# Performance work log

Measured on AMD Instinct MI355X. Metric: run time of the kernel, lower is better.

The kernel has to match this reference:

```python
import jax, jax.numpy as jnp
import numpy as np

B, P, D = 16, 512, 1024   # batch, num wordpieces, bert_dim (roberta-large)
W, T, E = 400, 32, 64     # num words, num triggers (spans), num entities (spans)
H = 600                   # hidden_num of role_idn_ffn


def _make_idxs(rng, b, m, n, max_len):
    # [start, end) intervals with 0 <= start < end <= n, sorted starts per row
    starts = np.sort(rng.integers(0, n - 1, size=(b, m)), axis=1)
    ends = np.minimum(starts + rng.integers(1, max_len + 1, size=(b, m)), n)
    ends = np.maximum(ends, starts + 1)
    return np.stack([starts, ends], axis=-1).astype(np.int32)


def setup_inputs() -> dict:
    key = jax.random.key(0)
    k1, k2, k3 = jax.random.split(key, 3)
    rng = np.random.default_rng(0)
    return {
        "piece_reprs": jax.random.normal(k1, (B, P, D), dtype=jnp.float32),
        "word_idxs": jnp.asarray(_make_idxs(rng, B, W, P, 4)),
        "trigger_idxs": jnp.asarray(_make_idxs(rng, B, T, W, 8)),
        "entity_idxs": jnp.asarray(_make_idxs(rng, B, E, W, 12)),
        "W0": jax.random.normal(k2, (4 * D, H), dtype=jnp.float32) * 0.02,
        "b0": jnp.zeros((H,), dtype=jnp.float32),
        "W1": jax.random.normal(k3, (H, 2), dtype=jnp.float32) * 0.02,
        "b1": jnp.zeros((2,), dtype=jnp.float32),
    }


def _segment_mean(x, idxs):
    """Mean of x[b, start:end] per interval. x: [B,N,Dm], idxs: [B,M,2] -> [B,M,Dm].
    Vectorized replacement of the nested-loop slice+mean via inclusive prefix sums."""
    cs = jnp.concatenate([jnp.zeros_like(x[:, :1]), jnp.cumsum(x, axis=1)], axis=1)  # [B,N+1,Dm]
    s = jnp.take_along_axis(cs, idxs[:, :, 0:1], axis=1)  # [B,M,Dm]
    e = jnp.take_along_axis(cs, idxs[:, :, 1:2], axis=1)  # [B,M,Dm]
    lens = (idxs[:, :, 1] - idxs[:, :, 0]).astype(x.dtype)[:, :, None]
    return (e - s) / lens


def reference(piece_reprs, word_idxs, trigger_idxs, entity_idxs, W0, b0, W1, b1):
    # encode(): wordpiece -> word averaging (compute_word_reps_avg)
    word_reprs = _segment_mean(piece_reprs, word_idxs)          # [B, W, D]
    # scores(): span mean pooling (compute_span_reprs)
    trig = _segment_mean(word_reprs, trigger_idxs)              # [B, T, D]
    ent = _segment_mean(word_reprs, entity_idxs)                # [B, E, D]
    b, t, d = trig.shape
    e = ent.shape[1]
    # compute_binary_reprs: all (trigger, entity) pairs, trigger index varies slowly
    t_rep = jnp.broadcast_to(trig[:, :, None, :], (b, t, e, d)).reshape(b, t * e, d)
    e_rep = jnp.broadcast_to(ent[:, None, :, :], (b, t, e, d)).reshape(b, t * e, d)
    role = jnp.concatenate([t_rep, e_rep, t_rep * e_rep, jnp.abs(t_rep - e_rep)], axis=-1)  # [B,T*E,4D]
    # role_idn_ffn: Linears([4D, H, 2]) with relu between layers (dropout=0 at eval)
    h = jax.nn.relu(role @ W0 + b0)
    return h @ W1 + b1                                          # [B, T*E, 2]
```

## Files before the change

kernel.cpp:

```cpp
#include <hip/hip_runtime.h>
#include <cstddef>
#include <cstdint>

typedef float f32x4 __attribute__((ext_vector_type(4)));
typedef __bf16 bf16x8 __attribute__((ext_vector_type(8)));

constexpr int NB = 16;
constexpr int NP = 512;
constexpr int ND = 1024;
constexpr int NW = 400;
constexpr int NT = 32;
constexpr int NE = 64;
constexpr int NH = 600;
constexpr int IMGP = 128 * 64;
constexpr int IMGQ = 320 * 32;
constexpr int PREZ_N = NB * NT * NH + NB * NE * NH;

__device__ inline bf16x8 pack8(float a0, float a1, float a2, float a3,
                               float a4, float a5, float a6, float a7) {
    bf16x8 v;
    v[0] = (__bf16)a0; v[1] = (__bf16)a1; v[2] = (__bf16)a2; v[3] = (__bf16)a3;
    v[4] = (__bf16)a4; v[5] = (__bf16)a5; v[6] = (__bf16)a6; v[7] = (__bf16)a7;
    return v;
}

__device__ inline void dma16(const void* g, void* l) {
    __builtin_amdgcn_global_load_lds(
        (const __attribute__((address_space(1))) uint32_t*)g,
        (__attribute__((address_space(3))) uint32_t*)l, 16, 0, 0);
}

#define LGKM_BARRIER() \
    asm volatile("s_waitcnt lgkmcnt(0)\n\ts_barrier" ::: "memory")

template <int MAXW>
__device__ inline float4 span_mean_cols(const float* __restrict__ pbase,
                                        const int* __restrict__ wrow,
                                        int s, int e) {
    int nw = e - s;
    int ps[MAXW], pe[MAXW];
#pragma unroll
    for (int w = 0; w < MAXW; ++w) {
        bool act = w < nw;
        int ww = s + w;
        ps[w] = act ? wrow[2 * ww] : 0;
        pe[w] = act ? wrow[2 * ww + 1] : 0;
    }
    float4 acc = make_float4(0.f, 0.f, 0.f, 0.f);
#pragma unroll
    for (int cb = 0; cb < MAXW; cb += 4) {
#pragma unroll
        for (int w = cb; w < cb + 4; ++w) {
            float4 wa = make_float4(0.f, 0.f, 0.f, 0.f);
#pragma unroll
            for (int p = 0; p < 4; ++p) {
                if (ps[w] + p < pe[w]) {
                    float4 v =
                        *(const float4*)(pbase + (size_t)(ps[w] + p) * ND);
                    wa.x += v.x; wa.y += v.y; wa.z += v.z; wa.w += v.w;
                }
            }
            if (pe[w] > ps[w]) {
                float wi = 1.0f / (float)(pe[w] - ps[w]);
                acc.x += wa.x * wi; acc.y += wa.y * wi;
                acc.z += wa.z * wi; acc.w += wa.w * wi;
            }
        }
    }
    return acc;
}

__global__ __launch_bounds__(256) void prep_kernel(
    const float* __restrict__ piece, const int* __restrict__ widx,
    const int* __restrict__ tidx, const int* __restrict__ eidx,
    const float* __restrict__ W0, __bf16* __restrict__ W0pre,
    __bf16* __restrict__ W0pair, float* __restrict__ trig,
    float* __restrict__ ent, float* __restrict__ prez,
    float* __restrict__ out, int out_size) {
    __shared__ float T[32][132];
    int id = blockIdx.x;
    int t = threadIdx.x;
    if (id < NB * (NT + NE)) {
        const int* idx;
        float* outp;
        int b;
        bool is_trig = id < NB * NT;
        if (is_trig) {
            b = id / NT; idx = tidx + id * 2; outp = trig + (size_t)id * ND;
        } else {
            int id2 = id - NB * NT;
            b = id2 / NE; idx = eidx + id2 * 2; outp = ent + (size_t)id2 * ND;
        }
        int s = idx[0], e = idx[1];
        int col = t * 4;
        const int* wrow = widx + b * NW * 2;
        const float* pbase = piece + (size_t)b * NP * ND + col;
        float4 acc = is_trig ? span_mean_cols<8>(pbase, wrow, s, e)
                             : span_mean_cols<12>(pbase, wrow, s, e);
        float inv = 1.0f / (float)(e - s);
        acc.x *= inv; acc.y *= inv; acc.z *= inv; acc.w *= inv;
        *(float4*)(outp + col) = acc;
    } else if (id < NB * (NT + NE) + 704) {
        int bid = id - NB * (NT + NE);
        if (bid < 160) {
            int kb = bid & 31, nc = bid >> 5;
            __bf16* img = W0pre + ((size_t)nc * 32 + kb) * IMGP;
#pragma unroll
            for (int h = 0; h < 2; ++h) {
                {
                    int kl = t >> 3;
                    int n0 = (t & 7) * 16;
                    int kg = kb * 64 + h * 32 + kl;
                    const float* src = W0 + (size_t)kg * NH + nc * 128 + n0;
#pragma unroll
                    for (int g = 0; g < 4; ++g) {
                        int n = nc * 128 + n0 + g * 4;
                        float4 v = (n < NH) ? *(const float4*)(src + g * 4)
                                            : make_float4(0.f, 0.f, 0.f, 0.f);
                        *(float4*)&T[kl][n0 + g * 4] = v;
                    }
                }
                __syncthreads();
#pragma unroll
                for (int s = 0; s < 2; ++s) {
                    int idx = s * 256 + t;
                    int row = idx >> 2, cl = idx & 3, c = h * 4 + cl;
                    bf16x8 v = pack8(T[cl * 8 + 0][row], T[cl * 8 + 1][row],
                                     T[cl * 8 + 2][row], T[cl * 8 + 3][row],
                                     T[cl * 8 + 4][row], T[cl * 8 + 5][row],
                                     T[cl * 8 + 6][row], T[cl * 8 + 7][row]);
                    *(bf16x8*)&img[row * 64 + ((c ^ (row & 7)) << 3)] = v;
                }
                __syncthreads();
            }
        } else if (bid < 672) {
            int e = bid - 160;
            int it = e & 63, nc = (e >> 6) & 1, zz = e >> 7;
            float (*Tp)[84] = reinterpret_cast<float(*)[84]>(&T[0][0]);
            {
                int kidx = t >> 3, part = t & 7;
                int korig = (kidx < 16) ? (2048 + it * 16 + kidx)
                                        : (3072 + it * 16 + (kidx - 16));
                const float* src = W0 + (size_t)korig * NH;
#pragma unroll
                for (int g = 0; g < 10; ++g) {
                    int n = nc * 320 + zz * 80 + part * 10 + g;
                    Tp[kidx][part * 10 + g] = (n < NH) ? src[n] : 0.0f;
                }
            }
            __syncthreads();
            __bf16* img = W0pair + ((size_t)nc * 64 + it) * IMGQ;
#pragma unroll
            for (int s = 0; s < 2; ++s) {
                int idx = s * 256 + t;
                if (idx < 320) {
                    int rloc = idx >> 2, c = idx & 3;
                    bf16x8 v = pack8(Tp[c * 8 + 0][rloc], Tp[c * 8 + 1][rloc],
                                     Tp[c * 8 + 2][rloc], Tp[c * 8 + 3][rloc],
                                     Tp[c * 8 + 4][rloc], Tp[c * 8 + 5][rloc],
                                     Tp[c * 8 + 6][rloc], Tp[c * 8 + 7][rloc]);
                    int rg = zz * 80 + rloc;
                    int slot = ((rg >> 1) + c) & 3;
                    *(bf16x8*)&img[rg * 32 + slot * 8] = v;
                }
            }
        } else {
            int j = ((bid - 672) * 256 + t) * 8;
            float4 z = make_float4(0.f, 0.f, 0.f, 0.f);
            if (j + 8 <= out_size) {
                *(float4*)(out + j) = z;
                *(float4*)(out + j + 4) = z;
            }
        }
    } else {
        int id2 = id - (NB * (NT + NE) + 704);
        int j = (id2 * 256 + t) * 8;
        float4 z = make_float4(0.f, 0.f, 0.f, 0.f);
        if (j + 8 <= PREZ_N) {
            *(float4*)(prez + j) = z;
            *(float4*)(prez + j + 4) = z;
        }
    }
}

__global__ __launch_bounds__(256) void pre_mfma_kernel(
    const float* __restrict__ trig, const float* __restrict__ ent,
    const __bf16* __restrict__ W0pre, float* __restrict__ pre_t,
    float* __restrict__ pre_e) {
    __shared__ __bf16 As[2][64 * 64];
    __shared__ __bf16 Bs[3][64 * 64];
    int mt8 = blockIdx.x, ntile = blockIdx.y, kz = blockIdx.z;
    const float* A;
    float* C;
    int kbofs, mbase;
    if (mt8 < 8) { A = trig; C = pre_t; kbofs = 0;  mbase = mt8 * 64; }
    else         { A = ent;  C = pre_e; kbofs = 16; mbase = (mt8 - 8) * 64; }
    int tid = threadIdx.x;
    int lane = tid & 63, w = tid >> 6, rw = w & 1, cw = w >> 1;
    int q = lane >> 4, l15 = lane & 15, sa = l15 & 7;
    int nc = ntile >> 1, half = ntile & 1;
    const __bf16* imgbase =
        W0pre + ((size_t)nc * 32 + kbofs) * IMGP + half * 4096;
    int ar = tid >> 2, seg = tid & 3;
    f32x4 acc[2][2] = {};
    float4 av[4];

    auto dma_bb = [&](int it, int buf) {
        const __bf16* img = imgbase + (size_t)(kz * 8 + it) * IMGP;
#pragma unroll
        for (int i = 0; i < 2; ++i) {
            int idx = i * 4 + w;
            dma16(img + idx * 512 + lane * 8, (__bf16*)Bs[buf] + idx * 512);
        }
    };
    auto load_a = [&](int it) {
        const float* src = A + (size_t)(mbase + ar) * ND + (kz * 8 + it) * 64;
#pragma unroll
        for (int i = 0; i < 2; ++i) {
            int c = seg * 2 + i;
            av[i * 2]     = *(const float4*)(src + c * 8);
            av[i * 2 + 1] = *(const float4*)(src + c * 8 + 4);
        }
    };
    auto write_a = [&](int buf) {
#pragma unroll
        for (int i = 0; i < 2; ++i) {
            int c = seg * 2 + i;
            float4 a0 = av[i * 2], a1 = av[i * 2 + 1];
            *(bf16x8*)&As[buf][ar * 64 + ((c ^ (ar & 7)) << 3)] =
                pack8(a0.x, a0.y, a0.z, a0.w, a1.x, a1.y, a1.z, a1.w);
        }
    };
    auto mfma_t = [&](int abuf, int bbuf) {
#pragma unroll
        for (int ks = 0; ks < 2; ++ks) {
            int coff = ((q ^ sa) ^ (ks << 2)) << 3;
            bf16x8 af[2];
#pragma unroll
            for (int mt = 0; mt < 2; ++mt)
                af[mt] = *(const bf16x8*)&As[abuf][(32 * rw + 16 * mt + l15) * 64 + coff];
#pragma unroll
            for (int nt = 0; nt < 2; ++nt) {
                bf16x8 bf = *(const bf16x8*)&Bs[bbuf][(32 * cw + 16 * nt + l15) * 64 + coff];
#pragma unroll
                for (int mt = 0; mt < 2; ++mt)
                    acc[mt][nt] = __builtin_amdgcn_mfma_f32_16x16x32_bf16(
                        af[mt], bf, acc[mt][nt], 0, 0, 0);
            }
        }
    };

    load_a(0);
    dma_bb(0, 0);
    dma_bb(1, 1);
    write_a(0);
    __syncthreads();

    int bc = 0, bp = 2;
    for (int it = 0; it < 8; ++it) {
        int acur = it & 1, anxt = acur ^ 1;
        if (it < 7) load_a(it + 1);
        if (it < 6) dma_bb(it + 2, bp);
        __builtin_amdgcn_s_setprio(1);
        mfma_t(acur, bc);
        __builtin_amdgcn_s_setprio(0);
        if (it < 7) write_a(anxt);
        LGKM_BARRIER();
        bc = (bc == 2) ? 0 : bc + 1;
        bp = (bp == 2) ? 0 : bp + 1;
    }

#pragma unroll
    for (int mt = 0; mt < 2; ++mt)
#pragma unroll
        for (int r = 0; r < 4; ++r) {
            float* crow =
                C + (size_t)(mbase + 32 * rw + 16 * mt + 4 * q + r) * NH;
#pragma unroll
            for (int nt = 0; nt < 2; ++nt) {
                int n = ntile * 64 + 32 * cw + 16 * nt + l15;
                if (n < NH) atomicAdd(&crow[n], acc[mt][nt][r]);
            }
        }
}

__global__ __launch_bounds__(256, 2) void pair_mfma_kernel(
    const float* __restrict__ trig, const float* __restrict__ ent,
    const __bf16* __restrict__ W0pair, const float* __restrict__ b0,
    const float* __restrict__ pre_t, const float* __restrict__ pre_e,
    const float* __restrict__ W1, const float* __restrict__ b1,
    float* __restrict__ out) {
    __shared__ __bf16 Xs[2][128 * 32];
    __shared__ __bf16 Bs[2][320 * 32];
    __shared__ __bf16 Ts[2048];
    int b = blockIdx.x, tp = blockIdx.y, nc = blockIdx.z;
    int tid = threadIdx.x;
    int lane = tid & 63, w = tid >> 6, rw = w & 1, cw = w >> 1;
    int q = lane >> 4, l15 = lane & 15;
    int xr = tid >> 1, xh = tid & 1;
    const float* t0row = trig + (size_t)(b * NT + tp * 2) * ND;
    const float* erow = ent + (size_t)(b * NE + (xr & 63)) * ND;
    const __bf16* imgbase = W0pair + (size_t)nc * 64 * IMGQ;
    f32x4 acc[4][10] = {};
    float4 ef4[2];

    auto dma_b = [&](int it, int buf) {
        const __bf16* img = imgbase + (size_t)it * IMGQ + w * 2560;
        __bf16* lds = &Bs[buf][w * 2560];
#pragma unroll
        for (int i = 0; i < 5; ++i)
            dma16(img + i * 512 + lane * 8, lds + i * 512);
    };
    auto load_e = [&](int it) {
        const float* er = erow + it * 16 + xh * 8;
        ef4[0] = *(const float4*)er;
        ef4[1] = *(const float4*)(er + 4);
    };
    auto write_x = [&](int it, int buf) {
        bf16x8 tv = *(const bf16x8*)&Ts[(xr >> 6) * 1024 + it * 16 + xh * 8];
        float tf[8], ef[8];
#pragma unroll
        for (int j = 0; j < 8; ++j) tf[j] = (float)tv[j];
        ef[0] = ef4[0].x; ef[1] = ef4[0].y; ef[2] = ef4[0].z; ef[3] = ef4[0].w;
        ef[4] = ef4[1].x; ef[5] = ef4[1].y; ef[6] = ef4[1].z; ef[7] = ef4[1].w;
        int sp = (((xr >> 1) + xh) & 3) * 8;
        int sd = (((xr >> 1) + 2 + xh) & 3) * 8;
        __bf16* xb = &Xs[buf][xr * 32];
        *(bf16x8*)(xb + sp) = pack8(
            tf[0] * ef[0], tf[1] * ef[1], tf[2] * ef[2], tf[3] * ef[3],
            tf[4] * ef[4], tf[5] * ef[5], tf[6] * ef[6], tf[7] * ef[7]);
        *(bf16x8*)(xb + sd) = pack8(
            fabsf(tf[0] - ef[0]), fabsf(tf[1] - ef[1]),
            fabsf(tf[2] - ef[2]), fabsf(tf[3] - ef[3]),
            fabsf(tf[4] - ef[4]), fabsf(tf[5] - ef[5]),
            fabsf(tf[6] - ef[6]), fabsf(tf[7] - ef[7]));
    };
    auto mfma_tile = [&](int buf) {
        const __bf16* X = Xs[buf];
        const __bf16* Bb = Bs[buf];
        bf16x8 af[4];
#pragma unroll
        for (int mt = 0; mt < 4; ++mt) {
            int r = 64 * rw + 16 * mt + l15;
            af[mt] = *(const bf16x8*)&X[r * 32 + (((r >> 1) + q) & 3) * 8];
        }
#pragma unroll
        for (int nt = 0; nt < 10; ++nt) {
            int r = 160 * cw + 16 * nt + l15;
            bf16x8 bv = *(const bf16x8*)&Bb[r * 32 + (((r >> 1) + q) & 3) * 8];
#pragma unroll
            for (int mt = 0; mt < 4; ++mt)
                acc[mt][nt] = __builtin_amdgcn_mfma_f32_16x16x32_bf16(
                    af[mt], bv, acc[mt][nt], 0, 0, 0);
        }
    };

    {
        int k0 = (tid & 127) * 8;
        const float* src = t0row + (tid >> 7) * ND + k0;
        float4 va = *(const float4*)src;
        float4 vb = *(const float4*)(src + 4);
        *(bf16x8*)&Ts[tid * 8] =
            pack8(va.x, va.y, va.z, va.w, vb.x, vb.y, vb.z, vb.w);
    }
    dma_b(0, 0);
    load_e(0);
    __syncthreads();
    write_x(0, 0);
    __syncthreads();

    for (int it = 0; it < 64; ++it) {
        int cur = it & 1, nxt = cur ^ 1;
        if (it < 63) {
            load_e(it + 1);
            dma_b(it + 1, nxt);
        }
        mfma_tile(cur);
        if (it < 63) write_x(it + 1, nxt);
        __syncthreads();
    }

    int tglob = b * NT + tp * 2 + rw;
    const float* preT = pre_t + (size_t)tglob * NH;
    float w10[10], w11[10], b0v[10], ptv[10];
    int nbase = nc * 320 + 160 * cw + l15;
#pragma unroll
    for (int nt = 0; nt < 10; ++nt) {
        int n = nbase + 16 * nt;
        bool v = n < NH;
        w10[nt] = v ? W1[2 * n] : 0.f;
        w11[nt] = v ? W1[2 * n + 1] : 0.f;
        b0v[nt] = v ? b0[n] : 0.f;
        ptv[nt] = v ? preT[n] : 0.f;
    }
    float b10 = b1[0], b11 = b1[1];
    bool lead = (l15 == 0);
    bool addb = (nc == 0) && (cw == 0);
#pragma unroll
    for (int mt = 0; mt < 4; ++mt) {
#pragma unroll
        for (int r = 0; r < 4; ++r) {
            int e = 16 * mt + 4 * q + r;
            const float* preE = pre_e + (size_t)(b * NE + e) * NH;
            float s0 = 0.f, s1 = 0.f;
#pragma unroll
            for (int nt = 0; nt < 10; ++nt) {
                int n = nbase + 16 * nt;
                float pe = (n < NH) ? preE[n] : 0.f;
                float h = acc[mt][nt][r] + ptv[nt] + pe + b0v[nt];
                h = fmaxf(h, 0.f);
                s0 += h * w10[nt];
                s1 += h * w11[nt];
            }
#pragma unroll
            for (int m = 8; m >= 1; m >>= 1) {
                s0 += __shfl_xor(s0, m);
                s1 += __shfl_xor(s1, m);
            }
            if (lead) {
                if (addb) { s0 += b10; s1 += b11; }
                float* o = out + ((size_t)(tglob * NE + e)) * 2;
                atomicAdd(o, s0);
                atomicAdd(o + 1, s1);
            }
        }
    }
}

extern "C" void kernel_launch(void* const* d_in, const int* in_sizes, int n_in,
                              void* d_out, int out_size, void* d_ws,
                              size_t ws_size, hipStream_t stream) {
    const float* piece = (const float*)d_in[0];
    const int* widx = (const int*)d_in[1];
    const int* tidx = (const int*)d_in[2];
    const int* eidx = (const int*)d_in[3];
    const float* W0 = (const float*)d_in[4];
    const float* b0 = (const float*)d_in[5];
    const float* W1 = (const float*)d_in[6];
    const float* b1 = (const float*)d_in[7];
    float* out = (float*)d_out;

    float* ws = (float*)d_ws;
    float* trig = ws;
    float* ent = trig + (size_t)NB * NT * ND;
    float* pre_t = ent + (size_t)NB * NE * ND;
    float* pre_e = pre_t + (size_t)NB * NT * NH;
    __bf16* W0pre = (__bf16*)(pre_e + (size_t)NB * NE * NH);
    __bf16* W0pair = W0pre + (size_t)5 * 32 * IMGP;

    int nprep = NB * (NT + NE) + 704 + (PREZ_N / 2048);
    prep_kernel<<<nprep, 256, 0, stream>>>(piece, widx, tidx, eidx, W0, W0pre,
                                           W0pair, trig, ent, pre_t, out,
                                           out_size);
    pre_mfma_kernel<<<dim3(24, 10, 2), 256, 0, stream>>>(trig, ent, W0pre,
                                                         pre_t, pre_e);
    pair_mfma_kernel<<<dim3(16, 16, 2), 256, 0, stream>>>(
        trig, ent, W0pair, b0, pre_t, pre_e, W1, b1, out);
}
```

Baseline: 216.7 us.

## Deepen entity-load prefetch, keep trigger tile in fp32 LDS, raise MFMA priority

Unrolls the main K loop by two with fixed buffer indices. Entity rows are now prefetched two iterations ahead through alternating register sets, and each X tile is written before the MFMA phase instead of after it, giving global loads more time to land. The trigger rows are kept in LDS as fp32 rather than bf16, which doubles that LDS footprint but drops the conversion step. MFMA sections are wrapped in s_setprio to favour matrix issue. Risks include higher register and LDS pressure, which could lower occupancy at 2 blocks per CU, and changed rounding of the trigger values before the product.

```diff
diff --git a/kernel.cpp b/kernel.cpp
--- a/kernel.cpp
+++ b/kernel.cpp
@@ -292,7 +292,7 @@
     float* __restrict__ out) {
     __shared__ __bf16 Xs[2][128 * 32];
     __shared__ __bf16 Bs[2][320 * 32];
-    __shared__ __bf16 Ts[2048];
+    __shared__ float Ts[2048];
     int b = blockIdx.x, tp = blockIdx.y, nc = blockIdx.z;
     int tid = threadIdx.x;
     int lane = tid & 63, w = tid >> 6, rw = w & 1, cw = w >> 1;
@@ -302,7 +302,7 @@
     const float* erow = ent + (size_t)(b * NE + (xr & 63)) * ND;
     const __bf16* imgbase = W0pair + (size_t)nc * 64 * IMGQ;
     f32x4 acc[4][10] = {};
-    float4 ef4[2];
+    float4 efA0, efA1, efB0, efB1;
 
     auto dma_b = [&](int it, int buf) {
         const __bf16* img = imgbase + (size_t)it * IMGQ + w * 2560;
@@ -311,18 +311,25 @@
         for (int i = 0; i < 5; ++i)
             dma16(img + i * 512 + lane * 8, lds + i * 512);
     };
-    auto load_e = [&](int it) {
+    auto load_eA = [&](int it) {
         const float* er = erow + it * 16 + xh * 8;
-        ef4[0] = *(const float4*)er;
-        ef4[1] = *(const float4*)(er + 4);
-    };
-    auto write_x = [&](int it, int buf) {
-        bf16x8 tv = *(const bf16x8*)&Ts[(xr >> 6) * 1024 + it * 16 + xh * 8];
+        efA0 = *(const float4*)er;
+        efA1 = *(const float4*)(er + 4);
+    };
+    auto load_eB = [&](int it) {
+        const float* er = erow + it * 16 + xh * 8;
+        efB0 = *(const float4*)er;
+        efB1 = *(const float4*)(er + 4);
+    };
+    auto write_x = [&](int it, int buf, float4 e0, float4 e1) {
+        const float* tsp = &Ts[(xr >> 6) * 1024 + it * 16 + xh * 8];
+        float4 t0 = *(const float4*)tsp;
+        float4 t1 = *(const float4*)(tsp + 4);
         float tf[8], ef[8];
-#pragma unroll
-        for (int j = 0; j < 8; ++j) tf[j] = (float)tv[j];
-        ef[0] = ef4[0].x; ef[1] = ef4[0].y; ef[2] = ef4[0].z; ef[3] = ef4[0].w;
-        ef[4] = ef4[1].x; ef[5] = ef4[1].y; ef[6] = ef4[1].z; ef[7] = ef4[1].w;
+        tf[0] = t0.x; tf[1] = t0.y; tf[2] = t0.z; tf[3] = t0.w;
+        tf[4] = t1.x; tf[5] = t1.y; tf[6] = t1.z; tf[7] = t1.w;
+        ef[0] = e0.x; ef[1] = e0.y; ef[2] = e0.z; ef[3] = e0.w;
+        ef[4] = e1.x; ef[5] = e1.y; ef[6] = e1.z; ef[7] = e1.w;
         int sp = (((xr >> 1) + xh) & 3) * 8;
         int sd = (((xr >> 1) + 2 + xh) & 3) * 8;
         __bf16* xb = &Xs[buf][xr * 32];
@@ -344,6 +351,7 @@
             int r = 64 * rw + 16 * mt + l15;
             af[mt] = *(const bf16x8*)&X[r * 32 + (((r >> 1) + q) & 3) * 8];
         }
+        __builtin_amdgcn_s_setprio(1);
 #pragma unroll
         for (int nt = 0; nt < 10; ++nt) {
             int r = 160 * cw + 16 * nt + l15;
@@ -353,30 +361,39 @@
                 acc[mt][nt] = __builtin_amdgcn_mfma_f32_16x16x32_bf16(
                     af[mt], bv, acc[mt][nt], 0, 0, 0);
         }
+        __builtin_amdgcn_s_setprio(0);
     };
 
     {
         int k0 = (tid & 127) * 8;
-        const float* src = t0row + (tid >> 7) * ND + k0;
+        int row = tid >> 7;
+        const float* src = t0row + row * ND + k0;
         float4 va = *(const float4*)src;
         float4 vb = *(const float4*)(src + 4);
-        *(bf16x8*)&Ts[tid * 8] =
-            pack8(va.x, va.y, va.z, va.w, vb.x, vb.y, vb.z, vb.w);
-    }
+        *(float4*)&Ts[row * 1024 + k0] = va;
+        *(float4*)&Ts[row * 1024 + k0 + 4] = vb;
+    }
+    load_eA(0);
     dma_b(0, 0);
-    load_e(0);
     __syncthreads();
-    write_x(0, 0);
+    load_eB(1);
+    write_x(0, 0, efA0, efA1);
     __syncthreads();
 
-    for (int it = 0; it < 64; ++it) {
-        int cur = it & 1, nxt = cur ^ 1;
-        if (it < 63) {
-            load_e(it + 1);
-            dma_b(it + 1, nxt);
-        }
-        mfma_tile(cur);
-        if (it < 63) write_x(it + 1, nxt);
+    for (int itp = 0; itp < 32; ++itp) {
+        int it0 = itp * 2;
+        int it1 = it0 + 1;
+        if (it0 < 62) load_eA(it0 + 2);
+        dma_b(it0 + 1, 1);
+        write_x(it0 + 1, 1, efB0, efB1);
+        mfma_tile(0);
+        __syncthreads();
+        if (it1 < 62) load_eB(it1 + 2);
+        if (it1 < 63) {
+            dma_b(it1 + 1, 0);
+            write_x(it1 + 1, 0, efA0, efA1);
+        }
+        mfma_tile(1);
         __syncthreads();
     }
 
```

New measurement: 206.0 us. 1.05x faster.
